# Kernel optimization log

Measured on AMD Instinct MI355X. Metric: run time of the kernel, lower is better.

Reference implementation:

```python
import jax, jax.numpy as jnp
import numpy as np

NQ = 14      # num_qubits
DEPTH = 6    # ansatz depth
DIM = 2 ** NQ

# Convention: flattened statevector index uses qubit 0 as the MOST significant bit
# (qubit q sits at bit position NQ-1-q). This matches building the state by
# successive kron with later qubits in lower bits.

def _bits(idx, q):
    return (idx >> (NQ - 1 - q)) & 1


def setup_inputs() -> dict:
    key = jax.random.key(0)
    k1, k2, k3 = jax.random.split(key, 3)
    x = jax.random.normal(k1, (512, NQ), dtype=jnp.float32)
    theta = jax.random.normal(k2, (NQ * DEPTH,), dtype=jnp.float32) * 0.1
    head_w = jax.random.normal(k3, (2, NQ), dtype=jnp.float32) * 0.3
    head_b = jnp.zeros((2,), dtype=jnp.float32)
    return {"x": x, "theta": theta, "head_w": head_w, "head_b": head_b}


def _simulate(x, theta):
    B = x.shape[0]
    half = 0.5 * x
    c = jnp.cos(half).astype(jnp.complex64)          # (B, NQ)
    s = jnp.sin(half).astype(jnp.complex64)
    # RX(x_q) applied to |0>^n gives a product state: kron of [cos(x/2), -i sin(x/2)]
    state = jnp.ones((B, 1), dtype=jnp.complex64)
    for q in range(NQ):
        v = jnp.stack([c[:, q], (-1j) * s[:, q]], axis=-1)   # (B, 2)
        state = (state[:, :, None] * v[:, None, :]).reshape(B, -1)
    # state: (B, DIM)

    idx = jnp.arange(DIM)
    bits = jnp.stack([_bits(idx, q) for q in range(NQ)], axis=0)     # (NQ, DIM)
    # CZ chain on (q, q+1): diagonal phase (-1)^(sum of adjacent bit ANDs)
    cz_parity = jnp.sum(bits[:-1] * bits[1:], axis=0) % 2
    cz_sign = jnp.where(cz_parity == 1, -1.0, 1.0).astype(jnp.complex64)  # (DIM,)

    for d in range(DEPTH):
        for q in range(NQ):
            t = 0.5 * theta[d * NQ + q]
            ct, st = jnp.cos(t), jnp.sin(t)
            G = jnp.stack([jnp.stack([ct, -st]), jnp.stack([st, ct])]).astype(jnp.complex64)
            sr = state.reshape(B, 2 ** q, 2, -1)   # qubit q at this axis
            state = jnp.einsum('ab,iqbr->iqar', G, sr).reshape(B, DIM)
        state = state * cz_sign[None, :]

    probs = state.real ** 2 + state.imag ** 2       # (B, DIM)
    zsign = (1.0 - 2.0 * bits).astype(jnp.float32)  # (NQ, DIM), Z eigenvalues per qubit
    zexp = probs @ zsign.T                          # (B, NQ), index = our qubit label
    # Qiskit: observable i = 'I'*i + 'Z' + 'I'*(NQ-i-1) acts on qubit NQ-1-i
    return zexp[:, ::-1]


def reference(x, theta, head_w, head_b):
    exp_tensor = _simulate(x, theta)                # (B, NQ)
    logits = exp_tensor @ head_w.T + head_b         # (B, 2)
    return logits
```

## Files before the change

kernel.cpp:

```cpp
#include <hip/hip_runtime.h>
#include <math.h>

#define NQ 14
#define DEPTH 6
#define BLOCK 512
#define TS 528u

typedef _Float16 h16;
typedef h16 h4 __attribute__((ext_vector_type(4)));
typedef float f4 __attribute__((ext_vector_type(4)));

__global__ __launch_bounds__(BLOCK, 6) void qsim_kernel(
    const float* __restrict__ x, const float* __restrict__ theta,
    const float* __restrict__ head_w, const float* __restrict__ head_b,
    float* __restrict__ out)
{
  extern __shared__ __align__(16) char sbuf[];
  __shared__ __align__(16) h16 Bm[24][256];
  __shared__ float2 gtab[DEPTH * NQ];
  __shared__ float wA[2][16], wB[2][16], wC[2][4], wD[2][4], wE[2][4];
  __shared__ float xc[NQ], xs[NQ];
  __shared__ float redbuf[16];

  const int t = threadIdx.x;
  const int b = blockIdx.x >> 1;
  const int comp = blockIdx.x & 1;
  const int lane = t & 63;
  const int w = t >> 6;
  const int m = lane & 15;
  const int kg = lane >> 4;

  if (t < DEPTH * NQ) {
    int d = t / NQ, bit = t - d * NQ;
    float hg = 0.5f * theta[d * NQ + (13 - bit)];
    gtab[t] = make_float2(cosf(hg), sinf(hg));
  } else if (t >= 128 && t < 160) {
    int o = (t - 128) >> 4, v = t & 15; float s = 0.f;
    #pragma unroll
    for (int i = 0; i < 4; ++i) s += ((v >> i) & 1) ? -head_w[o*NQ+i] : head_w[o*NQ+i];
    wA[o][v] = s;
  } else if (t >= 160 && t < 192) {
    int o = (t - 160) >> 4, v = t & 15; float s = 0.f;
    #pragma unroll
    for (int i = 0; i < 4; ++i) s += ((v >> i) & 1) ? -head_w[o*NQ+8+i] : head_w[o*NQ+8+i];
    wB[o][v] = s;
  } else if (t >= 192 && t < 200) {
    int o = (t - 192) >> 2, v = t & 3;
    float s = ((v & 1) ? -head_w[o*NQ+4] : head_w[o*NQ+4])
            + ((v & 2) ? -head_w[o*NQ+5] : head_w[o*NQ+5]);
    wC[o][v] = s;
  } else if (t >= 200 && t < 208) {
    int o = (t - 200) >> 2, v = t & 3;
    float s = ((v & 1) ? -head_w[o*NQ+6] : head_w[o*NQ+6])
            + ((v & 2) ? -head_w[o*NQ+7] : head_w[o*NQ+7]);
    wD[o][v] = s;
  } else if (t >= 208 && t < 216) {
    int o = (t - 208) >> 2, v = t & 3;
    float s = ((v & 1) ? -head_w[o*NQ+12] : head_w[o*NQ+12])
            + ((v & 2) ? -head_w[o*NQ+13] : head_w[o*NQ+13]);
    wE[o][v] = s;
  } else if (t >= 224 && t < 224 + NQ) {
    int bit = t - 224;
    float h = 0.5f * x[b * NQ + (13 - bit)];
    xc[bit] = cosf(h); xs[bit] = sinf(h);
  }
  __syncthreads();

  #pragma unroll
  for (int i = 0; i < 12; ++i) {
    int e = t + (i << 9);
    int pid = e >> 8, n = (e >> 4) & 15, k = e & 15;
    int d = pid >> 2, p = pid & 3;
    float val;
    if (p < 3) {
      val = 1.f;
      #pragma unroll
      for (int j = 0; j < 4; ++j) {
        float2 g = gtab[d * NQ + 4 * p + j];
        val *= ((n >> j) & 1) ? (((k >> j) & 1) ? g.x : g.y)
                              : (((k >> j) & 1) ? -g.y : g.x);
      }
      if (d >= 1) {
        int s = ((k & (k >> 1)) ^ ((k >> 1) & (k >> 2)) ^ ((k >> 2) & (k >> 3))) & 1;
        if (s) val = -val;
        if ((n & 1) && (k & 8)) val = -val;
      }
    } else {
      if ((((n ^ k) >> 2) & 3) != 0) val = 0.f;
      else {
        float2 gA = gtab[d * NQ + 12], gB = gtab[d * NQ + 13];
        float f0 = (n & 1) ? ((k & 1) ? gA.x : gA.y) : ((k & 1) ? -gA.y : gA.x);
        float f1 = ((n >> 1) & 1) ? (((k >> 1) & 1) ? gB.x : gB.y)
                                  : (((k >> 1) & 1) ? -gB.y : gB.x);
        val = f0 * f1;
        if (d >= 1 && (k & (k >> 1) & 1)) val = -val;
      }
    }
    Bm[pid][n * 16 + k] = (h16)val;
  }

  {
    float Mt = 1.f;
    #pragma unroll
    for (int p = 5; p < 14; ++p) Mt *= ((t >> (p - 5)) & 1) ? xs[p] : xc[p];
    const int pct = __popc((unsigned)t);
    uint32_t base = (uint32_t)(t >> 3) * TS + (uint32_t)((2 * t) & 15) * 32;
    #pragma unroll
    for (int g = 0; g < 4; ++g) {
      union { h16 h[8]; uint4 u; } pk;
      #pragma unroll
      for (int i = 0; i < 8; ++i) {
        int j = g * 8 + i;
        float mm = Mt;
        #pragma unroll
        for (int p = 0; p < 5; ++p) mm *= ((j >> p) & 1) ? xs[p] : xc[p];
        int e = (pct + __popc((unsigned)j)) & 3;
        float v = (comp == 0) ? ((e == 0) ? mm : ((e == 2) ? -mm : 0.f))
                              : ((e == 1) ? -mm : ((e == 3) ? mm : 0.f));
        pk.h[i] = (h16)v;
      }
      *(uint4*)(sbuf + base + (uint32_t)(g >> 1) * 32 + (uint32_t)(g & 1) * 16) = pk.u;
    }
  }
  __syncthreads();

  const uint32_t raA = (uint32_t)w * (8 * TS) + (uint32_t)m * 32 + (uint32_t)kg * 8;
  const uint32_t raB = (uint32_t)((w & 1) * 8 + 16 * (w >> 1)) * TS
                     + (uint32_t)m * 32 + (uint32_t)kg * 8;
  const uint32_t wbase = (uint32_t)m * TS + ((uint32_t)(w >> 1) + 4u * (uint32_t)kg) * 32
                       + (uint32_t)((w & 1) * 16);
  const uint32_t gfo = (uint32_t)(m * 16 + kg * 4) * 2;

  float l0 = 0.f, l1 = 0.f;

  auto do_half = [&](uint32_t rbase, h4 gB, h4 gA, bool last) {
    h4 av[8];
    #pragma unroll
    for (int jt = 0; jt < 8; ++jt)
      av[jt] = *(const h4*)(sbuf + rbase + (uint32_t)jt * TS);
    uint32_t qk[8][2];
    float bs0 = 0.f, bs1 = 0.f, we0[4], we1[4];
    if (last) {
      bs0 = wB[0][m] + wC[0][w >> 1] + wD[0][kg];
      bs1 = wB[1][m] + wC[1][w >> 1] + wD[1][kg];
      #pragma unroll
      for (int j = 0; j < 4; ++j) { we0[j] = wE[0][j]; we1[j] = wE[1][j]; }
    }
    #pragma unroll
    for (int jt = 0; jt < 8; ++jt) {
      f4 acc = {0.f, 0.f, 0.f, 0.f};
      acc = __builtin_amdgcn_mfma_f32_16x16x16f16(av[jt], gB, acc, 0, 0, 0);
      union { h16 h[4]; h4 v; uint32_t d[2]; } c1;
      c1.h[0] = (h16)acc[0]; c1.h[1] = (h16)acc[1];
      c1.h[2] = (h16)acc[2]; c1.h[3] = (h16)acc[3];
      f4 acc2 = {0.f, 0.f, 0.f, 0.f};
      acc2 = __builtin_amdgcn_mfma_f32_16x16x16f16(gA, c1.v, acc2, 0, 0, 0);
      if (!last) {
        union { h16 h[4]; uint32_t d[2]; } c2;
        c2.h[0] = (h16)acc2[0]; c2.h[1] = (h16)acc2[1];
        c2.h[2] = (h16)acc2[2]; c2.h[3] = (h16)acc2[3];
        qk[jt][0] = c2.d[0]; qk[jt][1] = c2.d[1];
      } else {
        float wt0 = wA[0][(w & 1) * 8 + jt], wt1 = wA[1][(w & 1) * 8 + jt];
        #pragma unroll
        for (int j = 0; j < 4; ++j) {
          float pr = acc2[j] * acc2[j];
          l0 += pr * (bs0 + wt0 + we0[j]);
          l1 += pr * (bs1 + wt1 + we1[j]);
        }
      }
    }
    if (!last) {
      __syncthreads();
      #pragma unroll
      for (int r = 0; r < 4; ++r) {
        uint32_t o[4];
        #pragma unroll
        for (int q = 0; q < 4; ++q) {
          uint32_t lo = qk[2 * q][r >> 1], hi = qk[2 * q + 1][r >> 1];
          o[q] = (r & 1) ? ((lo >> 16) | (hi & 0xffff0000u))
                         : ((lo & 0xffffu) | (hi << 16));
        }
        *(uint4*)(sbuf + wbase + (uint32_t)r * (16 * TS)) =
            make_uint4(o[0], o[1], o[2], o[3]);
      }
      __syncthreads();
    }
  };

  #pragma unroll 1
  for (int d = 0; d < DEPTH; ++d) {
    const char* base = (const char*)&Bm[d * 4 + 0][0];
    h4 g0f = *(const h4*)(base + gfo);
    h4 g1f = *(const h4*)(base + 512 + gfo);
    h4 g2f = *(const h4*)(base + 1024 + gfo);
    h4 g3f = *(const h4*)(base + 1536 + gfo);
    do_half(raA, g0f, g1f, false);
    do_half(raB, g2f, g3f, d == DEPTH - 1);
  }

  #pragma unroll
  for (int off = 32; off > 0; off >>= 1) {
    l0 += __shfl_xor(l0, off);
    l1 += __shfl_xor(l1, off);
  }
  if (lane == 0) { redbuf[w] = l0; redbuf[8 + w] = l1; }
  __syncthreads();
  if (t == 0) {
    float s0 = 0.f, s1 = 0.f;
    #pragma unroll
    for (int i = 0; i < 8; ++i) { s0 += redbuf[i]; s1 += redbuf[8 + i]; }
    if (comp == 0) { s0 += head_b[0]; s1 += head_b[1]; }
    atomicAdd(&out[b * 2 + 0], s0);
    atomicAdd(&out[b * 2 + 1], s1);
  }
}

extern "C" void kernel_launch(void* const* d_in, const int* in_sizes, int n_in,
                              void* d_out, int out_size, void* d_ws, size_t ws_size,
                              hipStream_t stream) {
    const float* x      = (const float*)d_in[0];
    const float* theta  = (const float*)d_in[1];
    const float* head_w = (const float*)d_in[2];
    const float* head_b = (const float*)d_in[3];
    float* outp = (float*)d_out;
    const int batch = in_sizes[0] / NQ;
    hipMemsetAsync(outp, 0, (size_t)out_size * sizeof(float), stream);
    qsim_kernel<<<batch * 2, BLOCK, 33856, stream>>>(x, theta, head_w, head_b, outp);
}
```

Before: 61.90 us.

## Hoist gate-matrix and head-weight table construction into a separate prep kernel

Moves the theta-dependent gate matrices (Bm) and head-weight sign tables out of the per-batch kernel into a single-block prep kernel that writes them to workspace. The main kernel then loads gate fragments from global memory with a one-depth-ahead register prefetch and no longer needs the 12 KB Bm shared array, which frees shared memory for higher occupancy (launch bounds raised to 8). In exchange it adds a second kernel launch, a dependency between the two launches, and global-memory loads on the critical path of each depth step.

```diff
diff --git a/kernel.cpp b/kernel.cpp
--- a/kernel.cpp
+++ b/kernel.cpp
@@ -5,67 +5,41 @@
 #define DEPTH 6
 #define BLOCK 512
 #define TS 528u
+#define BUFSZ 33792u
 
 typedef _Float16 h16;
 typedef h16 h4 __attribute__((ext_vector_type(4)));
 typedef float f4 __attribute__((ext_vector_type(4)));
 
-__global__ __launch_bounds__(BLOCK, 6) void qsim_kernel(
-    const float* __restrict__ x, const float* __restrict__ theta,
-    const float* __restrict__ head_w, const float* __restrict__ head_b,
-    float* __restrict__ out)
+__global__ __launch_bounds__(512, 1) void prep_kernel(
+    const float* __restrict__ theta, const float* __restrict__ head_w,
+    h16* __restrict__ BmG, float* __restrict__ wtab)
 {
-  extern __shared__ __align__(16) char sbuf[];
-  __shared__ __align__(16) h16 Bm[24][256];
   __shared__ float2 gtab[DEPTH * NQ];
-  __shared__ float wA[2][16], wB[2][16], wC[2][4], wD[2][4], wE[2][4];
-  __shared__ float xc[NQ], xs[NQ];
-  __shared__ float redbuf[16];
-
   const int t = threadIdx.x;
-  const int b = blockIdx.x >> 1;
-  const int comp = blockIdx.x & 1;
-  const int lane = t & 63;
-  const int w = t >> 6;
-  const int m = lane & 15;
-  const int kg = lane >> 4;
-
   if (t < DEPTH * NQ) {
     int d = t / NQ, bit = t - d * NQ;
     float hg = 0.5f * theta[d * NQ + (13 - bit)];
     gtab[t] = make_float2(cosf(hg), sinf(hg));
-  } else if (t >= 128 && t < 160) {
-    int o = (t - 128) >> 4, v = t & 15; float s = 0.f;
-    #pragma unroll
-    for (int i = 0; i < 4; ++i) s += ((v >> i) & 1) ? -head_w[o*NQ+i] : head_w[o*NQ+i];
-    wA[o][v] = s;
-  } else if (t >= 160 && t < 192) {
-    int o = (t - 160) >> 4, v = t & 15; float s = 0.f;
-    #pragma unroll
-    for (int i = 0; i < 4; ++i) s += ((v >> i) & 1) ? -head_w[o*NQ+8+i] : head_w[o*NQ+8+i];
-    wB[o][v] = s;
-  } else if (t >= 192 && t < 200) {
-    int o = (t - 192) >> 2, v = t & 3;
-    float s = ((v & 1) ? -head_w[o*NQ+4] : head_w[o*NQ+4])
-            + ((v & 2) ? -head_w[o*NQ+5] : head_w[o*NQ+5]);
-    wC[o][v] = s;
-  } else if (t >= 200 && t < 208) {
-    int o = (t - 200) >> 2, v = t & 3;
-    float s = ((v & 1) ? -head_w[o*NQ+6] : head_w[o*NQ+6])
-            + ((v & 2) ? -head_w[o*NQ+7] : head_w[o*NQ+7]);
-    wD[o][v] = s;
-  } else if (t >= 208 && t < 216) {
-    int o = (t - 208) >> 2, v = t & 3;
-    float s = ((v & 1) ? -head_w[o*NQ+12] : head_w[o*NQ+12])
-            + ((v & 2) ? -head_w[o*NQ+13] : head_w[o*NQ+13]);
-    wE[o][v] = s;
-  } else if (t >= 224 && t < 224 + NQ) {
-    int bit = t - 224;
-    float h = 0.5f * x[b * NQ + (13 - bit)];
-    xc[bit] = cosf(h); xs[bit] = sinf(h);
-  }
-  __syncthreads();
-
+  }
+  if (t < 88) {
+    int o, v; float s = 0.f;
+    if (t < 32) { o = t >> 4; v = t & 15;
+      #pragma unroll
+      for (int i = 0; i < 4; ++i) s += ((v>>i)&1) ? -head_w[o*NQ+i] : head_w[o*NQ+i];
+    } else if (t < 64) { o = (t-32) >> 4; v = t & 15;
+      #pragma unroll
+      for (int i = 0; i < 4; ++i) s += ((v>>i)&1) ? -head_w[o*NQ+8+i] : head_w[o*NQ+8+i];
+    } else if (t < 72) { o = (t-64) >> 2; v = t & 3;
+      s = ((v&1)?-head_w[o*NQ+4]:head_w[o*NQ+4]) + ((v&2)?-head_w[o*NQ+5]:head_w[o*NQ+5]);
+    } else if (t < 80) { o = (t-72) >> 2; v = t & 3;
+      s = ((v&1)?-head_w[o*NQ+6]:head_w[o*NQ+6]) + ((v&2)?-head_w[o*NQ+7]:head_w[o*NQ+7]);
+    } else { o = (t-80) >> 2; v = t & 3;
+      s = ((v&1)?-head_w[o*NQ+12]:head_w[o*NQ+12]) + ((v&2)?-head_w[o*NQ+13]:head_w[o*NQ+13]);
+    }
+    wtab[t] = s;
+  }
+  __syncthreads();
   #pragma unroll
   for (int i = 0; i < 12; ++i) {
     int e = t + (i << 9);
@@ -96,8 +70,35 @@
         if (d >= 1 && (k & (k >> 1) & 1)) val = -val;
       }
     }
-    Bm[pid][n * 16 + k] = (h16)val;
-  }
+    BmG[pid * 256 + n * 16 + k] = (h16)val;
+  }
+}
+
+__global__ __launch_bounds__(BLOCK, 8) void qsim_kernel(
+    const float* __restrict__ x, const h16* __restrict__ BmG,
+    const float* __restrict__ wtabG, const float* __restrict__ head_b,
+    float* __restrict__ out)
+{
+  extern __shared__ __align__(16) char sbuf[];
+  __shared__ float wtab[88];
+  __shared__ float xc[NQ], xs[NQ];
+  __shared__ float redbuf[16];
+
+  const int t = threadIdx.x;
+  const int b = blockIdx.x >> 1;
+  const int comp = blockIdx.x & 1;
+  const int lane = t & 63;
+  const int w = t >> 6;
+  const int m = lane & 15;
+  const int kg = lane >> 4;
+
+  if (t < 88) wtab[t] = wtabG[t];
+  if (t >= 128 && t < 128 + NQ) {
+    int bit = t - 128;
+    float h = 0.5f * x[b * NQ + (13 - bit)];
+    xc[bit] = cosf(h); xs[bit] = sinf(h);
+  }
+  __syncthreads();
 
   {
     float Mt = 1.f;
@@ -129,7 +130,6 @@
                      + (uint32_t)m * 32 + (uint32_t)kg * 8;
   const uint32_t wbase = (uint32_t)m * TS + ((uint32_t)(w >> 1) + 4u * (uint32_t)kg) * 32
                        + (uint32_t)((w & 1) * 16);
-  const uint32_t gfo = (uint32_t)(m * 16 + kg * 4) * 2;
 
   float l0 = 0.f, l1 = 0.f;
 
@@ -139,12 +139,10 @@
     for (int jt = 0; jt < 8; ++jt)
       av[jt] = *(const h4*)(sbuf + rbase + (uint32_t)jt * TS);
     uint32_t qk[8][2];
-    float bs0 = 0.f, bs1 = 0.f, we0[4], we1[4];
+    float bs0 = 0.f, bs1 = 0.f;
     if (last) {
-      bs0 = wB[0][m] + wC[0][w >> 1] + wD[0][kg];
-      bs1 = wB[1][m] + wC[1][w >> 1] + wD[1][kg];
-      #pragma unroll
-      for (int j = 0; j < 4; ++j) { we0[j] = wE[0][j]; we1[j] = wE[1][j]; }
+      bs0 = wtab[32 + m] + wtab[64 + (w >> 1)] + wtab[72 + kg];
+      bs1 = wtab[48 + m] + wtab[68 + (w >> 1)] + wtab[76 + kg];
     }
     #pragma unroll
     for (int jt = 0; jt < 8; ++jt) {
@@ -161,12 +159,12 @@
         c2.h[2] = (h16)acc2[2]; c2.h[3] = (h16)acc2[3];
         qk[jt][0] = c2.d[0]; qk[jt][1] = c2.d[1];
       } else {
-        float wt0 = wA[0][(w & 1) * 8 + jt], wt1 = wA[1][(w & 1) * 8 + jt];
+        float wt0 = wtab[(w & 1) * 8 + jt], wt1 = wtab[16 + (w & 1) * 8 + jt];
         #pragma unroll
         for (int j = 0; j < 4; ++j) {
           float pr = acc2[j] * acc2[j];
-          l0 += pr * (bs0 + wt0 + we0[j]);
-          l1 += pr * (bs1 + wt1 + we1[j]);
+          l0 += pr * (bs0 + wt0 + wtab[80 + j]);
+          l1 += pr * (bs1 + wt1 + wtab[84 + j]);
         }
       }
     }
@@ -188,15 +186,21 @@
     }
   };
 
+  const h16* fb = BmG + (m * 16 + kg * 4);
+  h4 c0 = *(const h4*)(fb +   0), c1 = *(const h4*)(fb + 256);
+  h4 c2 = *(const h4*)(fb + 512), c3 = *(const h4*)(fb + 768);
+
   #pragma unroll 1
   for (int d = 0; d < DEPTH; ++d) {
-    const char* base = (const char*)&Bm[d * 4 + 0][0];
-    h4 g0f = *(const h4*)(base + gfo);
-    h4 g1f = *(const h4*)(base + 512 + gfo);
-    h4 g2f = *(const h4*)(base + 1024 + gfo);
-    h4 g3f = *(const h4*)(base + 1536 + gfo);
-    do_half(raA, g0f, g1f, false);
-    do_half(raB, g2f, g3f, d == DEPTH - 1);
+    h4 n0 = {}, n1 = {}, n2 = {}, n3 = {};
+    if (d + 1 < DEPTH) {
+      const h16* nf = fb + (d + 1) * 1024;
+      n0 = *(const h4*)(nf +   0); n1 = *(const h4*)(nf + 256);
+      n2 = *(const h4*)(nf + 512); n3 = *(const h4*)(nf + 768);
+    }
+    do_half(raA, c0, c1, false);
+    do_half(raB, c2, c3, d == DEPTH - 1);
+    c0 = n0; c1 = n1; c2 = n2; c3 = n3;
   }
 
   #pragma unroll
@@ -224,7 +228,10 @@
     const float* head_w = (const float*)d_in[2];
     const float* head_b = (const float*)d_in[3];
     float* outp = (float*)d_out;
+    h16*  BmG   = (h16*)d_ws;
+    float* wtabG = (float*)((char*)d_ws + 12288);
     const int batch = in_sizes[0] / NQ;
     hipMemsetAsync(outp, 0, (size_t)out_size * sizeof(float), stream);
-    qsim_kernel<<<batch * 2, BLOCK, 33856, stream>>>(x, theta, head_w, head_b, outp);
+    prep_kernel<<<1, 512, 0, stream>>>(theta, head_w, BmG, wtabG);
+    qsim_kernel<<<batch * 2, BLOCK, BUFSZ, stream>>>(x, BmG, wtabG, head_b, outp);
 }
```

After: 56.97 us. 1.09x faster.
